# Kernel optimization log

Measured on AMD Instinct MI355X. Metric: run time of the kernel, lower is better.

The kernel has to match this reference:

```python
import jax, jax.numpy as jnp
import numpy as np

HIDDEN = 1024
MOE_INTER = 512
SHARED_INTER = 2048
N_EXPERTS = 32
TOP_K = 6
N_GROUP = 8
TOPK_GROUP = 4
ROUTED_SCALE = 2.5


def setup_inputs() -> dict:
    key = jax.random.key(0)
    ks = jax.random.split(key, 6)
    s = 0.02
    return {
        "hidden_states": jax.random.normal(ks[0], (2, 1024, HIDDEN), jnp.float32),
        "gate_w": jax.random.normal(ks[1], (N_EXPERTS, HIDDEN), jnp.float32) * s,
        "e_bias": jnp.zeros((N_EXPERTS,), jnp.float32),  # e_score_correction_bias (non-trainable)
        "up_w": jax.random.normal(ks[2], (N_EXPERTS, MOE_INTER, HIDDEN), jnp.float32) * s,
        "down_w": jax.random.normal(ks[3], (N_EXPERTS, HIDDEN, MOE_INTER), jnp.float32) * s,
        "shared_up_w": jax.random.normal(ks[4], (SHARED_INTER, HIDDEN), jnp.float32) * s,
        "shared_down_w": jax.random.normal(ks[5], (HIDDEN, SHARED_INTER), jnp.float32) * s,
    }


def _relu2(x):
    # Nemotron-H 'relu2' activation: relu(x)^2
    return jnp.square(jax.nn.relu(x))


def _router(x, gate_w, e_bias):
    # x: [T, H] -> topk_idx [T, K] (int), topk_w [T, K] (fp32)
    T = x.shape[0]
    logits = x.astype(jnp.float32) @ gate_w.astype(jnp.float32).T  # [T, E]
    scores = jax.nn.sigmoid(logits)
    sc = scores + e_bias[None, :]
    # group-limited routing: top-2 sum per group, keep topk_group groups
    g = sc.reshape(T, N_GROUP, N_EXPERTS // N_GROUP)
    group_scores = jax.lax.top_k(g, 2)[0].sum(-1)                  # [T, G]
    group_idx = jax.lax.top_k(group_scores, TOPK_GROUP)[1]         # [T, TG]
    group_mask = jnp.zeros_like(group_scores).at[jnp.arange(T)[:, None], group_idx].set(1.0)
    score_mask = jnp.repeat(group_mask, N_EXPERTS // N_GROUP, axis=1)  # [T, E]
    masked = jnp.where(score_mask > 0, sc, 0.0)
    topk_idx = jax.lax.stop_gradient(jax.lax.top_k(masked, TOP_K)[1])  # torch path is @no_grad
    topk_w = jnp.take_along_axis(scores, topk_idx, axis=1)         # gather from unbiased scores
    topk_w = topk_w / (topk_w.sum(-1, keepdims=True) + 1e-20)      # norm_topk_prob
    topk_w = topk_w * ROUTED_SCALE
    return topk_idx, topk_w


def reference(hidden_states, gate_w, e_bias, up_w, down_w, shared_up_w, shared_down_w):
    B, S, H = hidden_states.shape
    x = hidden_states.reshape(-1, H)  # [T, H]
    T = x.shape[0]
    topk_idx, topk_w = _router(x, gate_w, e_bias)
    # combine weights as dense [T, E] (scatter of top-k weights)
    combine = jnp.zeros((T, N_EXPERTS), topk_w.dtype).at[jnp.arange(T)[:, None], topk_idx].add(topk_w)
    # dense-masked expert compute; weight applied on intermediate (equivalent since
    # down_proj is linear with no bias): out = sum_e w_te * down_e(act(up_e(x)))
    h = _relu2(jnp.einsum('th,eih->tei', x, up_w))   # [T, E, I]
    h = h * combine[:, :, None]
    moe_out = jnp.einsum('tei,ehi->th', h, down_w)   # [T, H]
    shared = _relu2(x @ shared_up_w.T) @ shared_down_w.T
    return (moe_out + shared).reshape(B, S, H)


if __name__ == "__main__":
    out = reference(**setup_inputs())
    print(out.shape, out.dtype)
```

## Files before the change

kernel.cpp:

```cpp
#include <hip/hip_runtime.h>

typedef unsigned short u16;
typedef __bf16 bf16x8 __attribute__((ext_vector_type(8)));
typedef float f32x4 __attribute__((ext_vector_type(4)));
typedef u16 u16x8 __attribute__((ext_vector_type(8)));

#define T_TOK 2048
#define HID   1024
#define NEXP  32
#define IM    512
#define SI    2048
#define TOPK  6
#define PLAN_MAX 160

__device__ __forceinline__ u16 f2bf(float f){
  unsigned u = __float_as_uint(f);
  u += 0x7FFFu + ((u >> 16) & 1u);
  return (u16)(u >> 16);
}

__device__ __forceinline__ void gll16(const void* g, void* l){
  __builtin_amdgcn_global_load_lds((const __attribute__((address_space(1))) void*)g,
                                   (__attribute__((address_space(3))) void*)l, 16, 0, 0);
}

__device__ __forceinline__ u16x8 cvt2(float4 a, float4 b){
  u16x8 o;
  o[0] = f2bf(a.x); o[1] = f2bf(a.y); o[2] = f2bf(a.z); o[3] = f2bf(a.w);
  o[4] = f2bf(b.x); o[5] = f2bf(b.y); o[6] = f2bf(b.z); o[7] = f2bf(b.w);
  return o;
}

__global__ __launch_bounds__(256) void cvt_big_kernel(const float4* __restrict__ s1,
                                                      const float4* __restrict__ s2,
                                                      u16x8* __restrict__ d1,
                                                      u16x8* __restrict__ d2){
  long i = (long)blockIdx.x * 256 + threadIdx.x;
  const float4* s; u16x8* d;
  if (i < 2097152L){ s = s1; d = d1; }
  else             { s = s2; d = d2; i -= 2097152L; }
  float4 a = s[2*i], b = s[2*i+1];
  d[i] = cvt2(a, b);
}

__global__ __launch_bounds__(256) void cvt_small_kernel(const float4* __restrict__ s0,
                                                        const float4* __restrict__ s3,
                                                        const float4* __restrict__ s4,
                                                        u16x8* __restrict__ d0,
                                                        u16x8* __restrict__ d3,
                                                        u16x8* __restrict__ d4){
  long i = (long)blockIdx.x * 256 + threadIdx.x;
  const float4* s; u16x8* d;
  if      (i < 262144L){ s = s0; d = d0; }
  else if (i < 524288L){ s = s3; d = d3; i -= 262144L; }
  else                 { s = s4; d = d4; i -= 524288L; }
  float4 a = s[2*i], b = s[2*i+1];
  d[i] = cvt2(a, b);
}

__global__ __launch_bounds__(256) void router_kernel(const float* __restrict__ x,
                                                     const float* __restrict__ gate,
                                                     const float* __restrict__ ebias,
                                                     int* __restrict__ ce,
                                                     float* __restrict__ cw){
  int wave = threadIdx.x >> 6;
  int lane = threadIdx.x & 63;
  int t = blockIdx.x * 4 + wave;
  int e = lane & 31, half = lane >> 5;
  const float4* xv = (const float4*)(x + (size_t)t * HID);
  const float4* gv = (const float4*)(gate + (size_t)e * HID);
  double d0 = 0, d1 = 0, d2 = 0, d3 = 0;
  for (int i = half * 128; i < half * 128 + 128; i++){
    float4 a = xv[i], b = gv[i];
    d0 += (double)a.x * b.x; d1 += (double)a.y * b.y;
    d2 += (double)a.z * b.z; d3 += (double)a.w * b.w;
  }
  double acc = (d0 + d1) + (d2 + d3);
  acc += __shfl_xor(acc, 32);
  double score = 1.0 / (1.0 + exp(-acc));
  double sc = score + (double)ebias[e];
  double o1  = __shfl_xor(sc, 1);
  double hi  = fmax(sc, o1), lo = fmin(sc, o1);
  double ohi = __shfl_xor(hi, 2), olo = __shfl_xor(lo, 2);
  double gs  = (hi >= ohi) ? hi + fmax(lo, ohi) : ohi + fmax(olo, hi);
  int g = e >> 2;
  int rank = 0;
#pragma unroll
  for (int j = 0; j < 8; j++){
    double gj = __shfl(gs, j * 4);
    if (gj > gs || (gj == gs && j < g)) rank++;
  }
  double cur = (rank < 4) ? sc : 0.0;
  int sel_e[TOPK]; double sel_w[TOPK]; double wsum = 0.0;
#pragma unroll
  for (int k = 0; k < TOPK; k++){
    double bv = cur; int bi = lane;
#pragma unroll
    for (int m = 32; m >= 1; m >>= 1){
      double ov = __shfl_xor(bv, m); int oi = __shfl_xor(bi, m);
      if (ov > bv || (ov == bv && oi < bi)) { bv = ov; bi = oi; }
    }
    if ((bi & 31) == e) cur = -1e300;
    double ws = __shfl(score, bi);
    sel_e[k] = bi; sel_w[k] = ws; wsum += ws;
  }
  double scale = 2.5 / (wsum + 1e-20);
#pragma unroll
  for (int k = 0; k < TOPK; k++){
    if (lane == k){
      ce[t * TOPK + k] = sel_e[k] & 31;
      cw[t * TOPK + k] = (float)(sel_w[k] * scale);
    }
  }
}

__global__ __launch_bounds__(256) void build_kernel(const int* __restrict__ ce,
                                                    const float* __restrict__ cw,
                                                    int* __restrict__ cnt,
                                                    int* __restrict__ tok,
                                                    float* __restrict__ wl){
  int e = blockIdx.x;
  int tid = threadIdx.x, lane = tid & 63, wave = tid >> 6;
  __shared__ int wsum[4];
  int running = 0;
  for (int base = 0; base < T_TOK * TOPK; base += 256){
    int i = base + tid;
    bool m = (ce[i] == e);
    unsigned long long bal = __ballot(m);
    int woff = __popcll(bal & ((1ull << lane) - 1ull));
    if (lane == 0) wsum[wave] = __popcll(bal);
    __syncthreads();
    int wbase = 0;
#pragma unroll
    for (int wv = 0; wv < 4; wv++) if (wv < wave) wbase += wsum[wv];
    int btot = wsum[0] + wsum[1] + wsum[2] + wsum[3];
    if (m){
      int t = i / TOPK, k = i - t * TOPK;
      int pos = running + wbase + woff;
      tok[e * T_TOK + pos] = (t << 3) | k;
      wl[e * T_TOK + pos] = cw[i];
    }
    running += btot;
    __syncthreads();
  }
  if (tid == 0) cnt[e] = running;
}

__global__ __launch_bounds__(256) void plan_kernel(const int* __restrict__ cnt,
                                                   int* __restrict__ plan){
  int tid = threadIdx.x;
  if (tid < PLAN_MAX) plan[1 + tid] = -1;
  __syncthreads();
  if (tid == 0){
    int n = 0;
    for (int e = 0; e < NEXP; e++){
      int c = cnt[e];
      for (int tb = 0; tb < c; tb += 128) plan[1 + n++] = (tb << 8) | e;
    }
    plan[0] = n;
  }
}

__device__ __forceinline__ void gemm_core(
    const char* gA0, const char* gA1, const char* gB0, const char* gB1,
    u16* lA, u16* lB, int iters, int tid, int wrow, int wcol, int quad, int l16,
    f32x4 acc[4][4])
{
  char* dA0 = (char*)lA + tid*16;
  char* dA1 = (char*)lA + 4096 + tid*16;
  char* dB0 = (char*)lB + tid*16;
  char* dB1 = (char*)lB + 4096 + tid*16;
  for (int it = 0; it < iters; ++it){
    gll16(gA0, dA0); gll16(gA1, dA1);
    gll16(gB0, dB0); gll16(gB1, dB1);
    gA0 += 64; gA1 += 64; gB0 += 64; gB1 += 64;
    __syncthreads();
    bf16x8 af[4], bfr[4];
#pragma unroll
    for (int mt = 0; mt < 4; mt++) af[mt] = *(const bf16x8*)&lA[(wrow + mt*16 + l16)*32 + quad*8];
#pragma unroll
    for (int nt = 0; nt < 4; nt++) bfr[nt] = *(const bf16x8*)&lB[(wcol + nt*16 + l16)*32 + quad*8];
#pragma unroll
    for (int mt = 0; mt < 4; mt++)
#pragma unroll
      for (int nt = 0; nt < 4; nt++)
        acc[mt][nt] = __builtin_amdgcn_mfma_f32_16x16x32_bf16(af[mt], bfr[nt], acc[mt][nt], 0, 0, 0);
    __syncthreads();
  }
}

#define ACC_INIT f32x4 acc[4][4]; \
  _Pragma("unroll") for (int i_ = 0; i_ < 4; i_++) \
  _Pragma("unroll") for (int j_ = 0; j_ < 4; j_++) acc[i_][j_] = (f32x4){0.f,0.f,0.f,0.f};

__global__ __launch_bounds__(256) void sh_up_kernel(const u16* __restrict__ A,
                                                    const u16* __restrict__ B,
                                                    u16* __restrict__ C){
  __shared__ u16 lA[128*32], lB[128*32];
  int tid = threadIdx.x;
  int bm = blockIdx.x*128, bn = blockIdx.y*128;
  int lane = tid & 63, wave = tid >> 6, quad = lane >> 4, l16 = lane & 15;
  int wrow = (wave >> 1)*64, wcol = (wave & 1)*64;
  int srow = tid >> 2, sseg = (tid & 3)*16;
  const char* gA0 = (const char*)(A + (size_t)(bm + srow)*HID) + sseg;
  const char* gA1 = (const char*)(A + (size_t)(bm + 64 + srow)*HID) + sseg;
  const char* gB0 = (const char*)(B + (size_t)(bn + srow)*HID) + sseg;
  const char* gB1 = (const char*)(B + (size_t)(bn + 64 + srow)*HID) + sseg;
  ACC_INIT;
  gemm_core(gA0, gA1, gB0, gB1, lA, lB, HID/32, tid, wrow, wcol, quad, l16, acc);
#pragma unroll
  for (int mt = 0; mt < 4; mt++)
#pragma unroll
    for (int nt = 0; nt < 4; nt++)
#pragma unroll
      for (int r = 0; r < 4; r++){
        int m = bm + wrow + mt*16 + quad*4 + r;
        int n = bn + wcol + nt*16 + l16;
        float v = acc[mt][nt][r]; v = fmaxf(v, 0.f); v *= v;
        C[(size_t)m*SI + n] = f2bf(v);
      }
}

__global__ __launch_bounds__(256) void sh_down_kernel(const u16* __restrict__ A,
                                                      const u16* __restrict__ B,
                                                      float* __restrict__ C){
  __shared__ u16 lA[128*32], lB[128*32];
  int tid = threadIdx.x;
  int bm = blockIdx.x*128, bn = blockIdx.y*128;
  int lane = tid & 63, wave = tid >> 6, quad = lane >> 4, l16 = lane & 15;
  int wrow = (wave >> 1)*64, wcol = (wave & 1)*64;
  int srow = tid >> 2, sseg = (tid & 3)*16;
  const char* gA0 = (const char*)(A + (size_t)(bm + srow)*SI) + sseg;
  const char* gA1 = (const char*)(A + (size_t)(bm + 64 + srow)*SI) + sseg;
  const char* gB0 = (const char*)(B + (size_t)(bn + srow)*SI) + sseg;
  const char* gB1 = (const char*)(B + (size_t)(bn + 64 + srow)*SI) + sseg;
  ACC_INIT;
  gemm_core(gA0, gA1, gB0, gB1, lA, lB, SI/32, tid, wrow, wcol, quad, l16, acc);
#pragma unroll
  for (int mt = 0; mt < 4; mt++)
#pragma unroll
    for (int nt = 0; nt < 4; nt++)
#pragma unroll
      for (int r = 0; r < 4; r++){
        int m = bm + wrow + mt*16 + quad*4 + r;
        int n = bn + wcol + nt*16 + l16;
        C[(size_t)m*HID + n] = acc[mt][nt][r];
      }
}

__global__ __launch_bounds__(256) void expert_up_kernel(const u16* __restrict__ xb,
                                                        const u16* __restrict__ upb,
                                                        const int* __restrict__ cnt,
                                                        const int* __restrict__ tok,
                                                        const float* __restrict__ wl,
                                                        const int* __restrict__ plan,
                                                        u16* __restrict__ hws){
  int pv = plan[1 + blockIdx.x];
  if (pv < 0) return;
  int e = pv & 255;
  int tb = pv >> 8;
  int c = cnt[e];
  int bn = blockIdx.y * 128;
  const int* tl = tok + e * T_TOK;
  const float* wle = wl + e * T_TOK;
  __shared__ u16 lA[128*32], lB[128*32];
  int tid = threadIdx.x;
  int lane = tid & 63, wave = tid >> 6, quad = lane >> 4, l16 = lane & 15;
  int wrow = (wave >> 1)*64, wcol = (wave & 1)*64;
  int srow = tid >> 2, sseg = (tid & 3)*16;
  int s0 = tb + srow;      if (s0 > c-1) s0 = c-1;
  int s1 = tb + 64 + srow; if (s1 > c-1) s1 = c-1;
  int t0 = tl[s0] >> 3, t1 = tl[s1] >> 3;
  const char* gA0 = (const char*)(xb + (size_t)t0*HID) + sseg;
  const char* gA1 = (const char*)(xb + (size_t)t1*HID) + sseg;
  const u16* Bb = upb + (size_t)e * IM * HID;
  const char* gB0 = (const char*)(Bb + (size_t)(bn + srow)*HID) + sseg;
  const char* gB1 = (const char*)(Bb + (size_t)(bn + 64 + srow)*HID) + sseg;
  ACC_INIT;
  gemm_core(gA0, gA1, gB0, gB1, lA, lB, HID/32, tid, wrow, wcol, quad, l16, acc);
#pragma unroll
  for (int mt = 0; mt < 4; mt++)
#pragma unroll
    for (int r = 0; r < 4; r++){
      int s = tb + wrow + mt*16 + quad*4 + r;
      if (s < c){
        int code = tl[s];
        float w = wle[s];
        size_t hb = ((size_t)(code >> 3) * TOPK + (code & 7)) * IM;
#pragma unroll
        for (int nt = 0; nt < 4; nt++){
          float v = acc[mt][nt][r]; v = fmaxf(v, 0.f); v = v * v * w;
          hws[hb + bn + wcol + nt*16 + l16] = f2bf(v);
        }
      }
    }
}

__global__ __launch_bounds__(256) void expert_down_kernel(const u16* __restrict__ hws,
                                                          const u16* __restrict__ dnb,
                                                          const int* __restrict__ cnt,
                                                          const int* __restrict__ tok,
                                                          const int* __restrict__ plan,
                                                          float* __restrict__ out){
  int pv = plan[1 + blockIdx.x];
  if (pv < 0) return;
  int e = pv & 255;
  int tb = pv >> 8;
  int c = cnt[e];
  int bn = blockIdx.y * 128;
  const int* tl = tok + e * T_TOK;
  __shared__ u16 lA[128*32], lB[128*32];
  int tid = threadIdx.x;
  int lane = tid & 63, wave = tid >> 6, quad = lane >> 4, l16 = lane & 15;
  int wrow = (wave >> 1)*64, wcol = (wave & 1)*64;
  int srow = tid >> 2, sseg = (tid & 3)*16;
  int s0 = tb + srow;      if (s0 > c-1) s0 = c-1;
  int s1 = tb + 64 + srow; if (s1 > c-1) s1 = c-1;
  int c0 = tl[s0], c1 = tl[s1];
  const char* gA0 = (const char*)(hws + ((size_t)(c0 >> 3)*TOPK + (c0 & 7))*IM) + sseg;
  const char* gA1 = (const char*)(hws + ((size_t)(c1 >> 3)*TOPK + (c1 & 7))*IM) + sseg;
  const u16* Bb = dnb + (size_t)e * HID * IM;
  const char* gB0 = (const char*)(Bb + (size_t)(bn + srow)*IM) + sseg;
  const char* gB1 = (const char*)(Bb + (size_t)(bn + 64 + srow)*IM) + sseg;
  ACC_INIT;
  gemm_core(gA0, gA1, gB0, gB1, lA, lB, IM/32, tid, wrow, wcol, quad, l16, acc);
#pragma unroll
  for (int mt = 0; mt < 4; mt++)
#pragma unroll
    for (int r = 0; r < 4; r++){
      int s = tb + wrow + mt*16 + quad*4 + r;
      if (s < c){
        int code = tl[s];
        float* ob = out + (size_t)(code >> 3) * HID;
#pragma unroll
        for (int nt = 0; nt < 4; nt++)
          unsafeAtomicAdd(&ob[bn + wcol + nt*16 + l16], acc[mt][nt][r]);
      }
    }
}

extern "C" void kernel_launch(void* const* d_in, const int* in_sizes, int n_in,
                              void* d_out, int out_size, void* d_ws, size_t ws_size,
                              hipStream_t stream) {
  const float* x    = (const float*)d_in[0];
  const float* gate = (const float*)d_in[1];
  const float* eb   = (const float*)d_in[2];
  const float* upw  = (const float*)d_in[3];
  const float* dnw  = (const float*)d_in[4];
  const float* supw = (const float*)d_in[5];
  const float* sdnw = (const float*)d_in[6];
  float* out = (float*)d_out;

  char* w = (char*)d_ws;
  size_t o = 0;
  int*   cnt  = (int*)(w + o);   o += 1024;
  int*   plan = (int*)(w + o);   o += 1024;
  int*   ce   = (int*)(w + o);   o += (size_t)T_TOK * TOPK * 4;
  float* cw   = (float*)(w + o); o += (size_t)T_TOK * TOPK * 4;
  int*   tok  = (int*)(w + o);   o += (size_t)NEXP * T_TOK * 4;
  float* wl   = (float*)(w + o); o += (size_t)NEXP * T_TOK * 4;
  u16*   xb   = (u16*)(w + o);   o += (size_t)T_TOK * HID * 2;
  u16*   dnb  = (u16*)(w + o);   o += (size_t)NEXP * HID * IM * 2;
  u16*   hws  = (u16*)(w + o);   o += (size_t)T_TOK * TOPK * IM * 2;
  u16*   upb  = (u16*)(w + o);   o += (size_t)NEXP * IM * HID * 2;
  u16*   supb = (u16*)(w + o);   o += (size_t)SI * HID * 2;
  u16*   sdnb = (u16*)(w + o);   o += (size_t)HID * SI * 2;
  u16*   shh  = (u16*)(w + o);   o += (size_t)T_TOK * SI * 2;

  cvt_big_kernel<<<16384, 256, 0, stream>>>(
      (const float4*)upw, (const float4*)dnw, (u16x8*)upb, (u16x8*)dnb);
  cvt_small_kernel<<<3072, 256, 0, stream>>>(
      (const float4*)x, (const float4*)supw, (const float4*)sdnw,
      (u16x8*)xb, (u16x8*)supb, (u16x8*)sdnb);

  router_kernel<<<T_TOK/4, 256, 0, stream>>>(x, gate, eb, ce, cw);
  build_kernel<<<NEXP, 256, 0, stream>>>(ce, cw, cnt, tok, wl);
  plan_kernel<<<1, 256, 0, stream>>>(cnt, plan);

  sh_up_kernel<<<dim3(T_TOK/128, SI/128), 256, 0, stream>>>(xb, supb, shh);
  sh_down_kernel<<<dim3(T_TOK/128, HID/128), 256, 0, stream>>>(shh, sdnb, out);

  expert_up_kernel<<<dim3(PLAN_MAX, IM/128), 256, 0, stream>>>(xb, upb, cnt, tok, wl, plan, hws);
  expert_down_kernel<<<dim3(PLAN_MAX, HID/128), 256, 0, stream>>>(hws, dnb, cnt, tok, plan, out);
}
```

Measured before the change: 407.2 us.

## Double-buffer GEMM LDS tiles and merge shared/expert GEMMs into fused launches

The GEMM core now double-buffers its LDS tiles, issuing the next k-slice's global-to-LDS loads before the MFMAs on the current slice, and drops one barrier per iteration. The shared-expert and routed-expert up GEMMs are merged into one launch, and the two down GEMMs into another. The shared down path now accumulates into an output zeroed by a memset instead of storing to it. The small-tensor conversion is merged with the router into one kernel. Together these aim to hide load latency, cut launch count and fill the GPU better. The cost is doubled LDS use, which may lower occupancy, and extra atomic traffic on the shared down output.

```diff
diff --git a/kernel.cpp b/kernel.cpp
--- a/kernel.cpp
+++ b/kernel.cpp
@@ -43,39 +43,35 @@
   d[i] = cvt2(a, b);
 }
 
-__global__ __launch_bounds__(256) void cvt_small_kernel(const float4* __restrict__ s0,
-                                                        const float4* __restrict__ s3,
-                                                        const float4* __restrict__ s4,
-                                                        u16x8* __restrict__ d0,
-                                                        u16x8* __restrict__ d3,
-                                                        u16x8* __restrict__ d4){
-  long i = (long)blockIdx.x * 256 + threadIdx.x;
-  const float4* s; u16x8* d;
-  if      (i < 262144L){ s = s0; d = d0; }
-  else if (i < 524288L){ s = s3; d = d3; i -= 262144L; }
-  else                 { s = s4; d = d4; i -= 524288L; }
-  float4 a = s[2*i], b = s[2*i+1];
-  d[i] = cvt2(a, b);
-}
-
-__global__ __launch_bounds__(256) void router_kernel(const float* __restrict__ x,
-                                                     const float* __restrict__ gate,
-                                                     const float* __restrict__ ebias,
-                                                     int* __restrict__ ce,
-                                                     float* __restrict__ cw){
+__global__ __launch_bounds__(256) void cvt_small_router_kernel(
+    const float* __restrict__ x, const float4* __restrict__ s3, const float4* __restrict__ s4,
+    const float* __restrict__ gate, const float* __restrict__ ebias,
+    u16x8* __restrict__ d0, u16x8* __restrict__ d3, u16x8* __restrict__ d4,
+    int* __restrict__ ce, float* __restrict__ cw){
+  int blk = blockIdx.x;
+  if (blk >= 512){
+    long i = (long)(blk - 512) * 256 + threadIdx.x;
+    const float4* s; u16x8* d;
+    if      (i < 262144L){ s = (const float4*)x; d = d0; }
+    else if (i < 524288L){ s = s3; d = d3; i -= 262144L; }
+    else                 { s = s4; d = d4; i -= 524288L; }
+    float4 a = s[2*i], b = s[2*i+1];
+    d[i] = cvt2(a, b);
+    return;
+  }
   int wave = threadIdx.x >> 6;
   int lane = threadIdx.x & 63;
-  int t = blockIdx.x * 4 + wave;
+  int t = blk * 4 + wave;
   int e = lane & 31, half = lane >> 5;
   const float4* xv = (const float4*)(x + (size_t)t * HID);
   const float4* gv = (const float4*)(gate + (size_t)e * HID);
-  double d0 = 0, d1 = 0, d2 = 0, d3 = 0;
+  double d0a = 0, d1a = 0, d2a = 0, d3a = 0;
   for (int i = half * 128; i < half * 128 + 128; i++){
     float4 a = xv[i], b = gv[i];
-    d0 += (double)a.x * b.x; d1 += (double)a.y * b.y;
-    d2 += (double)a.z * b.z; d3 += (double)a.w * b.w;
-  }
-  double acc = (d0 + d1) + (d2 + d3);
+    d0a += (double)a.x * b.x; d1a += (double)a.y * b.y;
+    d2a += (double)a.z * b.z; d3a += (double)a.w * b.w;
+  }
+  double acc = (d0a + d1a) + (d2a + d3a);
   acc += __shfl_xor(acc, 32);
   double score = 1.0 / (1.0 + exp(-acc));
   double sc = score + (double)ebias[e];
@@ -166,177 +162,181 @@
     u16* lA, u16* lB, int iters, int tid, int wrow, int wcol, int quad, int l16,
     f32x4 acc[4][4])
 {
-  char* dA0 = (char*)lA + tid*16;
-  char* dA1 = (char*)lA + 4096 + tid*16;
-  char* dB0 = (char*)lB + tid*16;
-  char* dB1 = (char*)lB + 4096 + tid*16;
-  for (int it = 0; it < iters; ++it){
-    gll16(gA0, dA0); gll16(gA1, dA1);
-    gll16(gB0, dB0); gll16(gB1, dB1);
+  char* bA = (char*)lA + tid*16;
+  char* bB = (char*)lB + tid*16;
+  gll16(gA0, bA);  gll16(gA1, bA + 4096);
+  gll16(gB0, bB);  gll16(gB1, bB + 4096);
+  gA0 += 64; gA1 += 64; gB0 += 64; gB1 += 64;
+  __syncthreads();
+  unsigned cur = 0;
+  for (int it = 0; it < iters - 1; ++it){
+    unsigned nxt = cur ^ 1;
+    gll16(gA0, bA + nxt*8192);  gll16(gA1, bA + nxt*8192 + 4096);
+    gll16(gB0, bB + nxt*8192);  gll16(gB1, bB + nxt*8192 + 4096);
     gA0 += 64; gA1 += 64; gB0 += 64; gB1 += 64;
-    __syncthreads();
+    const u16* rA = lA + cur*4096;
+    const u16* rB = lB + cur*4096;
     bf16x8 af[4], bfr[4];
 #pragma unroll
-    for (int mt = 0; mt < 4; mt++) af[mt] = *(const bf16x8*)&lA[(wrow + mt*16 + l16)*32 + quad*8];
-#pragma unroll
-    for (int nt = 0; nt < 4; nt++) bfr[nt] = *(const bf16x8*)&lB[(wcol + nt*16 + l16)*32 + quad*8];
+    for (int mt = 0; mt < 4; mt++) af[mt]  = *(const bf16x8*)&rA[(wrow + mt*16 + l16)*32 + quad*8];
+#pragma unroll
+    for (int nt = 0; nt < 4; nt++) bfr[nt] = *(const bf16x8*)&rB[(wcol + nt*16 + l16)*32 + quad*8];
 #pragma unroll
     for (int mt = 0; mt < 4; mt++)
 #pragma unroll
       for (int nt = 0; nt < 4; nt++)
         acc[mt][nt] = __builtin_amdgcn_mfma_f32_16x16x32_bf16(af[mt], bfr[nt], acc[mt][nt], 0, 0, 0);
     __syncthreads();
-  }
+    cur = nxt;
+  }
+  const u16* rA = lA + cur*4096;
+  const u16* rB = lB + cur*4096;
+  bf16x8 af[4], bfr[4];
+#pragma unroll
+  for (int mt = 0; mt < 4; mt++) af[mt]  = *(const bf16x8*)&rA[(wrow + mt*16 + l16)*32 + quad*8];
+#pragma unroll
+  for (int nt = 0; nt < 4; nt++) bfr[nt] = *(const bf16x8*)&rB[(wcol + nt*16 + l16)*32 + quad*8];
+#pragma unroll
+  for (int mt = 0; mt < 4; mt++)
+#pragma unroll
+    for (int nt = 0; nt < 4; nt++)
+      acc[mt][nt] = __builtin_amdgcn_mfma_f32_16x16x32_bf16(af[mt], bfr[nt], acc[mt][nt], 0, 0, 0);
 }
 
 #define ACC_INIT f32x4 acc[4][4]; \
   _Pragma("unroll") for (int i_ = 0; i_ < 4; i_++) \
   _Pragma("unroll") for (int j_ = 0; j_ < 4; j_++) acc[i_][j_] = (f32x4){0.f,0.f,0.f,0.f};
 
-__global__ __launch_bounds__(256) void sh_up_kernel(const u16* __restrict__ A,
-                                                    const u16* __restrict__ B,
-                                                    u16* __restrict__ C){
-  __shared__ u16 lA[128*32], lB[128*32];
-  int tid = threadIdx.x;
-  int bm = blockIdx.x*128, bn = blockIdx.y*128;
-  int lane = tid & 63, wave = tid >> 6, quad = lane >> 4, l16 = lane & 15;
-  int wrow = (wave >> 1)*64, wcol = (wave & 1)*64;
-  int srow = tid >> 2, sseg = (tid & 3)*16;
-  const char* gA0 = (const char*)(A + (size_t)(bm + srow)*HID) + sseg;
-  const char* gA1 = (const char*)(A + (size_t)(bm + 64 + srow)*HID) + sseg;
-  const char* gB0 = (const char*)(B + (size_t)(bn + srow)*HID) + sseg;
-  const char* gB1 = (const char*)(B + (size_t)(bn + 64 + srow)*HID) + sseg;
-  ACC_INIT;
-  gemm_core(gA0, gA1, gB0, gB1, lA, lB, HID/32, tid, wrow, wcol, quad, l16, acc);
-#pragma unroll
-  for (int mt = 0; mt < 4; mt++)
-#pragma unroll
-    for (int nt = 0; nt < 4; nt++)
-#pragma unroll
-      for (int r = 0; r < 4; r++){
-        int m = bm + wrow + mt*16 + quad*4 + r;
-        int n = bn + wcol + nt*16 + l16;
-        float v = acc[mt][nt][r]; v = fmaxf(v, 0.f); v *= v;
-        C[(size_t)m*SI + n] = f2bf(v);
-      }
-}
-
-__global__ __launch_bounds__(256) void sh_down_kernel(const u16* __restrict__ A,
-                                                      const u16* __restrict__ B,
-                                                      float* __restrict__ C){
-  __shared__ u16 lA[128*32], lB[128*32];
-  int tid = threadIdx.x;
-  int bm = blockIdx.x*128, bn = blockIdx.y*128;
-  int lane = tid & 63, wave = tid >> 6, quad = lane >> 4, l16 = lane & 15;
-  int wrow = (wave >> 1)*64, wcol = (wave & 1)*64;
-  int srow = tid >> 2, sseg = (tid & 3)*16;
-  const char* gA0 = (const char*)(A + (size_t)(bm + srow)*SI) + sseg;
-  const char* gA1 = (const char*)(A + (size_t)(bm + 64 + srow)*SI) + sseg;
-  const char* gB0 = (const char*)(B + (size_t)(bn + srow)*SI) + sseg;
-  const char* gB1 = (const char*)(B + (size_t)(bn + 64 + srow)*SI) + sseg;
-  ACC_INIT;
-  gemm_core(gA0, gA1, gB0, gB1, lA, lB, SI/32, tid, wrow, wcol, quad, l16, acc);
-#pragma unroll
-  for (int mt = 0; mt < 4; mt++)
-#pragma unroll
-    for (int nt = 0; nt < 4; nt++)
-#pragma unroll
-      for (int r = 0; r < 4; r++){
-        int m = bm + wrow + mt*16 + quad*4 + r;
-        int n = bn + wcol + nt*16 + l16;
-        C[(size_t)m*HID + n] = acc[mt][nt][r];
-      }
-}
-
-__global__ __launch_bounds__(256) void expert_up_kernel(const u16* __restrict__ xb,
-                                                        const u16* __restrict__ upb,
-                                                        const int* __restrict__ cnt,
-                                                        const int* __restrict__ tok,
-                                                        const float* __restrict__ wl,
-                                                        const int* __restrict__ plan,
-                                                        u16* __restrict__ hws){
-  int pv = plan[1 + blockIdx.x];
-  if (pv < 0) return;
-  int e = pv & 255;
-  int tb = pv >> 8;
-  int c = cnt[e];
-  int bn = blockIdx.y * 128;
-  const int* tl = tok + e * T_TOK;
-  const float* wle = wl + e * T_TOK;
-  __shared__ u16 lA[128*32], lB[128*32];
+__global__ __launch_bounds__(256) void up_fused_kernel(
+    const u16* __restrict__ xb, const u16* __restrict__ supb, const u16* __restrict__ upb,
+    const int* __restrict__ cnt, const int* __restrict__ tok, const float* __restrict__ wl,
+    const int* __restrict__ plan, u16* __restrict__ shh, u16* __restrict__ hws){
+  __shared__ u16 lA[2*128*32], lB[2*128*32];
   int tid = threadIdx.x;
   int lane = tid & 63, wave = tid >> 6, quad = lane >> 4, l16 = lane & 15;
   int wrow = (wave >> 1)*64, wcol = (wave & 1)*64;
   int srow = tid >> 2, sseg = (tid & 3)*16;
-  int s0 = tb + srow;      if (s0 > c-1) s0 = c-1;
-  int s1 = tb + 64 + srow; if (s1 > c-1) s1 = c-1;
-  int t0 = tl[s0] >> 3, t1 = tl[s1] >> 3;
-  const char* gA0 = (const char*)(xb + (size_t)t0*HID) + sseg;
-  const char* gA1 = (const char*)(xb + (size_t)t1*HID) + sseg;
-  const u16* Bb = upb + (size_t)e * IM * HID;
-  const char* gB0 = (const char*)(Bb + (size_t)(bn + srow)*HID) + sseg;
-  const char* gB1 = (const char*)(Bb + (size_t)(bn + 64 + srow)*HID) + sseg;
-  ACC_INIT;
-  gemm_core(gA0, gA1, gB0, gB1, lA, lB, HID/32, tid, wrow, wcol, quad, l16, acc);
-#pragma unroll
-  for (int mt = 0; mt < 4; mt++)
-#pragma unroll
-    for (int r = 0; r < 4; r++){
-      int s = tb + wrow + mt*16 + quad*4 + r;
-      if (s < c){
-        int code = tl[s];
-        float w = wle[s];
-        size_t hb = ((size_t)(code >> 3) * TOPK + (code & 7)) * IM;
-#pragma unroll
-        for (int nt = 0; nt < 4; nt++){
-          float v = acc[mt][nt][r]; v = fmaxf(v, 0.f); v = v * v * w;
-          hws[hb + bn + wcol + nt*16 + l16] = f2bf(v);
+  int blk = blockIdx.x;
+  if (blk < 256){
+    int bm = (blk >> 4) * 128, bn = (blk & 15) * 128;
+    const char* gA0 = (const char*)(xb + (size_t)(bm + srow)*HID) + sseg;
+    const char* gA1 = (const char*)(xb + (size_t)(bm + 64 + srow)*HID) + sseg;
+    const char* gB0 = (const char*)(supb + (size_t)(bn + srow)*HID) + sseg;
+    const char* gB1 = (const char*)(supb + (size_t)(bn + 64 + srow)*HID) + sseg;
+    ACC_INIT;
+    gemm_core(gA0, gA1, gB0, gB1, lA, lB, HID/32, tid, wrow, wcol, quad, l16, acc);
+#pragma unroll
+    for (int mt = 0; mt < 4; mt++)
+#pragma unroll
+      for (int nt = 0; nt < 4; nt++)
+#pragma unroll
+        for (int r = 0; r < 4; r++){
+          int m = bm + wrow + mt*16 + quad*4 + r;
+          int n = bn + wcol + nt*16 + l16;
+          float v = acc[mt][nt][r]; v = fmaxf(v, 0.f); v *= v;
+          shh[(size_t)m*SI + n] = f2bf(v);
+        }
+  } else {
+    int eu = blk - 256;
+    int pv = plan[1 + (eu >> 2)];
+    if (pv < 0) return;
+    int e = pv & 255;
+    int tb = pv >> 8;
+    int c = cnt[e];
+    int bn = (eu & 3) * 128;
+    const int* tl = tok + e * T_TOK;
+    const float* wle = wl + e * T_TOK;
+    int s0 = tb + srow;      if (s0 > c-1) s0 = c-1;
+    int s1 = tb + 64 + srow; if (s1 > c-1) s1 = c-1;
+    int t0 = tl[s0] >> 3, t1 = tl[s1] >> 3;
+    const char* gA0 = (const char*)(xb + (size_t)t0*HID) + sseg;
+    const char* gA1 = (const char*)(xb + (size_t)t1*HID) + sseg;
+    const u16* Bb = upb + (size_t)e * IM * HID;
+    const char* gB0 = (const char*)(Bb + (size_t)(bn + srow)*HID) + sseg;
+    const char* gB1 = (const char*)(Bb + (size_t)(bn + 64 + srow)*HID) + sseg;
+    ACC_INIT;
+    gemm_core(gA0, gA1, gB0, gB1, lA, lB, HID/32, tid, wrow, wcol, quad, l16, acc);
+#pragma unroll
+    for (int mt = 0; mt < 4; mt++)
+#pragma unroll
+      for (int r = 0; r < 4; r++){
+        int s = tb + wrow + mt*16 + quad*4 + r;
+        if (s < c){
+          int code = tl[s];
+          float w = wle[s];
+          size_t hb = ((size_t)(code >> 3) * TOPK + (code & 7)) * IM;
+#pragma unroll
+          for (int nt = 0; nt < 4; nt++){
+            float v = acc[mt][nt][r]; v = fmaxf(v, 0.f); v = v * v * w;
+            hws[hb + bn + wcol + nt*16 + l16] = f2bf(v);
+          }
         }
       }
-    }
-}
-
-__global__ __launch_bounds__(256) void expert_down_kernel(const u16* __restrict__ hws,
-                                                          const u16* __restrict__ dnb,
-                                                          const int* __restrict__ cnt,
-                                                          const int* __restrict__ tok,
-                                                          const int* __restrict__ plan,
-                                                          float* __restrict__ out){
-  int pv = plan[1 + blockIdx.x];
-  if (pv < 0) return;
-  int e = pv & 255;
-  int tb = pv >> 8;
-  int c = cnt[e];
-  int bn = blockIdx.y * 128;
-  const int* tl = tok + e * T_TOK;
-  __shared__ u16 lA[128*32], lB[128*32];
+  }
+}
+
+__global__ __launch_bounds__(256) void down_fused_kernel(
+    const u16* __restrict__ shh, const u16* __restrict__ sdnb,
+    const u16* __restrict__ hws, const u16* __restrict__ dnb,
+    const int* __restrict__ cnt, const int* __restrict__ tok, const int* __restrict__ plan,
+    float* __restrict__ out){
+  __shared__ u16 lA[2*128*32], lB[2*128*32];
   int tid = threadIdx.x;
   int lane = tid & 63, wave = tid >> 6, quad = lane >> 4, l16 = lane & 15;
   int wrow = (wave >> 1)*64, wcol = (wave & 1)*64;
   int srow = tid >> 2, sseg = (tid & 3)*16;
-  int s0 = tb + srow;      if (s0 > c-1) s0 = c-1;
-  int s1 = tb + 64 + srow; if (s1 > c-1) s1 = c-1;
-  int c0 = tl[s0], c1 = tl[s1];
-  const char* gA0 = (const char*)(hws + ((size_t)(c0 >> 3)*TOPK + (c0 & 7))*IM) + sseg;
-  const char* gA1 = (const char*)(hws + ((size_t)(c1 >> 3)*TOPK + (c1 & 7))*IM) + sseg;
-  const u16* Bb = dnb + (size_t)e * HID * IM;
-  const char* gB0 = (const char*)(Bb + (size_t)(bn + srow)*IM) + sseg;
-  const char* gB1 = (const char*)(Bb + (size_t)(bn + 64 + srow)*IM) + sseg;
-  ACC_INIT;
-  gemm_core(gA0, gA1, gB0, gB1, lA, lB, IM/32, tid, wrow, wcol, quad, l16, acc);
-#pragma unroll
-  for (int mt = 0; mt < 4; mt++)
-#pragma unroll
-    for (int r = 0; r < 4; r++){
-      int s = tb + wrow + mt*16 + quad*4 + r;
-      if (s < c){
-        int code = tl[s];
-        float* ob = out + (size_t)(code >> 3) * HID;
-#pragma unroll
-        for (int nt = 0; nt < 4; nt++)
-          unsafeAtomicAdd(&ob[bn + wcol + nt*16 + l16], acc[mt][nt][r]);
+  int blk = blockIdx.x;
+  if (blk < 128){
+    int bm = (blk >> 3)*128, bn = (blk & 7)*128;
+    const char* gA0 = (const char*)(shh + (size_t)(bm + srow)*SI) + sseg;
+    const char* gA1 = (const char*)(shh + (size_t)(bm + 64 + srow)*SI) + sseg;
+    const char* gB0 = (const char*)(sdnb + (size_t)(bn + srow)*SI) + sseg;
+    const char* gB1 = (const char*)(sdnb + (size_t)(bn + 64 + srow)*SI) + sseg;
+    ACC_INIT;
+    gemm_core(gA0, gA1, gB0, gB1, lA, lB, SI/32, tid, wrow, wcol, quad, l16, acc);
+#pragma unroll
+    for (int mt = 0; mt < 4; mt++)
+#pragma unroll
+      for (int nt = 0; nt < 4; nt++)
+#pragma unroll
+        for (int r = 0; r < 4; r++){
+          int m = bm + wrow + mt*16 + quad*4 + r;
+          int n = bn + wcol + nt*16 + l16;
+          unsafeAtomicAdd(&out[(size_t)m*HID + n], acc[mt][nt][r]);
+        }
+  } else {
+    int eu = blk - 128;
+    int pv = plan[1 + (eu >> 3)];
+    if (pv < 0) return;
+    int e = pv & 255;
+    int tb = pv >> 8;
+    int c = cnt[e];
+    int bn = (eu & 7) * 128;
+    const int* tl = tok + e * T_TOK;
+    int s0 = tb + srow;      if (s0 > c-1) s0 = c-1;
+    int s1 = tb + 64 + srow; if (s1 > c-1) s1 = c-1;
+    int c0 = tl[s0], c1 = tl[s1];
+    const char* gA0 = (const char*)(hws + ((size_t)(c0 >> 3)*TOPK + (c0 & 7))*IM) + sseg;
+    const char* gA1 = (const char*)(hws + ((size_t)(c1 >> 3)*TOPK + (c1 & 7))*IM) + sseg;
+    const u16* Bb = dnb + (size_t)e * HID * IM;
+    const char* gB0 = (const char*)(Bb + (size_t)(bn + srow)*IM) + sseg;
+    const char* gB1 = (const char*)(Bb + (size_t)(bn + 64 + srow)*IM) + sseg;
+    ACC_INIT;
+    gemm_core(gA0, gA1, gB0, gB1, lA, lB, IM/32, tid, wrow, wcol, quad, l16, acc);
+#pragma unroll
+    for (int mt = 0; mt < 4; mt++)
+#pragma unroll
+      for (int r = 0; r < 4; r++){
+        int s = tb + wrow + mt*16 + quad*4 + r;
+        if (s < c){
+          int code = tl[s];
+          float* ob = out + (size_t)(code >> 3) * HID;
+#pragma unroll
+          for (int nt = 0; nt < 4; nt++)
+            unsafeAtomicAdd(&ob[bn + wcol + nt*16 + l16], acc[mt][nt][r]);
+        }
       }
-    }
+  }
 }
 
 extern "C" void kernel_launch(void* const* d_in, const int* in_sizes, int n_in,
@@ -369,17 +369,13 @@
 
   cvt_big_kernel<<<16384, 256, 0, stream>>>(
       (const float4*)upw, (const float4*)dnw, (u16x8*)upb, (u16x8*)dnb);
-  cvt_small_kernel<<<3072, 256, 0, stream>>>(
-      (const float4*)x, (const float4*)supw, (const float4*)sdnw,
-      (u16x8*)xb, (u16x8*)supb, (u16x8*)sdnb);
-
-  router_kernel<<<T_TOK/4, 256, 0, stream>>>(x, gate, eb, ce, cw);
+  cvt_small_router_kernel<<<3584, 256, 0, stream>>>(
+      x, (const float4*)supw, (const float4*)sdnw, gate, eb,
+      (u16x8*)xb, (u16x8*)supb, (u16x8*)sdnb, ce, cw);
   build_kernel<<<NEXP, 256, 0, stream>>>(ce, cw, cnt, tok, wl);
   plan_kernel<<<1, 256, 0, stream>>>(cnt, plan);
 
-  sh_up_kernel<<<dim3(T_TOK/128, SI/128), 256, 0, stream>>>(xb, supb, shh);
-  sh_down_kernel<<<dim3(T_TOK/128, HID/128), 256, 0, stream>>>(shh, sdnb, out);
-
-  expert_up_kernel<<<dim3(PLAN_MAX, IM/128), 256, 0, stream>>>(xb, upb, cnt, tok, wl, plan, hws);
-  expert_down_kernel<<<dim3(PLAN_MAX, HID/128), 256, 0, stream>>>(hws, dnb, cnt, tok, plan, out);
-}
+  up_fused_kernel<<<896, 256, 0, stream>>>(xb, supb, upb, cnt, tok, wl, plan, shh, hws);
+  hipMemsetAsync(out, 0, (size_t)T_TOK * HID * 4, stream);
+  down_fused_kernel<<<1408, 256, 0, stream>>>(shh, sdnb, hws, dnb, cnt, tok, plan, out);
+}
```

After: 369.6 us. 1.1x faster.
